# Kernel optimization log

Measured on AMD Instinct MI355X. Metric: run time of the kernel, lower is better.

## Reference

```python
import jax, jax.numpy as jnp
import numpy as np

N = 50000
NUM_FEATURES = 128
HIDDEN = 64
NUM_CLASSES = 32
K_HOPS = 4
E = 1600000
CST = 1e-05


def setup_inputs() -> dict:
    key = jax.random.key(0)
    ks = jax.random.split(key, 12)
    def lin(k, fan_in, fan_out):
        b = 1.0 / np.sqrt(fan_in)
        kw, kb = jax.random.split(k)
        W = jax.random.uniform(kw, (fan_in, fan_out), jnp.float32, -b, b)
        bias = jax.random.uniform(kb, (fan_out,), jnp.float32, -b, b)
        return W, bias
    W_in, b_in = lin(ks[0], NUM_FEATURES, HIDDEN)
    WQ, bQ = lin(ks[1], HIDDEN, HIDDEN)
    WK, bK = lin(ks[2], HIDDEN, HIDDEN)
    WV, bV = lin(ks[3], HIDDEN, NUM_CLASSES)
    return {
        'node_feat': jax.random.normal(ks[4], (N, NUM_FEATURES), jnp.float32),
        'W_in': W_in, 'b_in': b_in,
        'WQ': WQ, 'bQ': bQ,
        'WK': WK, 'bK': bK,
        'WV': WV, 'bV': bV,
        'hopwise': jnp.ones((K_HOPS + 1,), jnp.float32),
        'teleport': jnp.ones((1,), jnp.float32),
        'edge_index': jax.random.randint(ks[5], (2, E), 0, N, jnp.int64 if jax.config.jax_enable_x64 else jnp.int32),
    }


def reference(node_feat, W_in, b_in, WQ, bQ, WK, bK, WV, bV, hopwise, teleport, edge_index):
    n = node_feat.shape[0]
    row, col = edge_index[0], edge_index[1]
    # random-walk norm: deg over targets (col), inverted, indexed at sources (row)
    deg = jax.ops.segment_sum(jnp.ones_like(row, node_feat.dtype), col, num_segments=n)
    deg_inv = jnp.where(deg > 0, 1.0 / deg, 0.0)
    norm = deg_inv[row]  # [E]

    x = jax.nn.relu(node_feat @ W_in + b_in)          # [n, h]
    Q = 1.0 + jax.nn.elu(x @ WQ + bQ)                 # [n, h]
    Kf = 1.0 + jax.nn.elu(x @ WK + bK)                # [n, h]
    V = x @ WV + bV                                   # [n, c]
    M = jnp.einsum('ni,nj->nij', Kf, V)               # [n, h, c]

    # global attention (teleport) branch
    teleportM = jnp.sum(M, axis=0) / n                # [h, c]
    teleportK = jnp.sum(Kf, axis=0) / n               # [h]
    teleportH = jnp.einsum('ni,ij->nj', Q, teleportM)
    teleportC = jnp.einsum('ni,i->n', Q, teleportK)[:, None] + CST
    teleportH = teleportH / teleportC

    hidden = V * hopwise[0]
    for hop in range(K_HOPS):
        # edge gather -> weight -> scatter-sum (message passing)
        M = jax.ops.segment_sum(norm[:, None, None] * M[row], col, num_segments=n)
        Kf = jax.ops.segment_sum(norm[:, None] * Kf[row], col, num_segments=n)
        H = jnp.einsum('ni,nij->nj', Q, M)
        C = jnp.sum(Q * Kf, axis=-1, keepdims=True) + CST
        hidden = hidden + hopwise[hop + 1] * (H / C)

    hidden = hidden + teleport * teleportH
    return hidden
```

## Files before the change

### kernel.cpp

```cpp
#include <hip/hip_runtime.h>
#include <math.h>
#include <stdint.h>

#define NN 50000
#define FIN 128
#define HD 64
#define CD 32
#define EE 1600000
#define CSTV 1e-5f
#define NB 49

typedef unsigned short u16;
typedef unsigned int u32;
typedef unsigned char u8;
typedef unsigned int uv2 __attribute__((ext_vector_type(2)));
typedef unsigned int uv4 __attribute__((ext_vector_type(4)));
typedef float fv2 __attribute__((ext_vector_type(2)));

static __device__ __forceinline__ float b2f(u16 u){
  union { float f; u32 i; } v; v.i = ((u32)u) << 16; return v.f;
}
static __device__ __forceinline__ u16 f2b(float f){
  union { float f; u32 u; } v; v.f = f;
  u32 u = v.u;
  u32 r = (u + 0x7fffu + ((u >> 16) & 1u)) >> 16;
  return (u16)r;
}
static __device__ __forceinline__ float ldin(const void* p, size_t i, int isf){
  return isf ? ((const float*)p)[i] : b2f(((const u16*)p)[i]);
}

static __device__ __forceinline__ void dec8(u32 g, float* f){
  fv2 lo = __builtin_amdgcn_cvt_pk_f32_fp8(g, false);
  fv2 hi = __builtin_amdgcn_cvt_pk_f32_fp8(g, true);
  f[0] = lo.x; f[1] = lo.y; f[2] = hi.x; f[3] = hi.y;
}
static __device__ __forceinline__ u32 enc8(const float* f){
  u32 r = 0;
  r = __builtin_amdgcn_cvt_pk_fp8_f32(f[0], f[1], r, false);
  r = __builtin_amdgcn_cvt_pk_fp8_f32(f[2], f[3], r, true);
  return r;
}
template<int C>
static __device__ __forceinline__ void loadF8(const u8* __restrict__ p, float* f){
  if constexpr (C == 32){
    uint4 g0 = ((const uint4*)p)[0];
    uint4 g1 = ((const uint4*)p)[1];
    dec8(g0.x, f+0);  dec8(g0.y, f+4);  dec8(g0.z, f+8);  dec8(g0.w, f+12);
    dec8(g1.x, f+16); dec8(g1.y, f+20); dec8(g1.z, f+24); dec8(g1.w, f+28);
  } else if constexpr (C == 16){
    uint4 g = *(const uint4*)p;
    dec8(g.x, f+0); dec8(g.y, f+4); dec8(g.z, f+8); dec8(g.w, f+12);
  } else {
    uint2 g = *(const uint2*)p;
    dec8(g.x, f+0); dec8(g.y, f+4);
  }
}
template<int C>
static __device__ __forceinline__ void storeF8NT(u8* __restrict__ p, const float* f){
  if constexpr (C == 32){
    uv4 g0, g1;
    g0.x=enc8(f+0);  g0.y=enc8(f+4);  g0.z=enc8(f+8);  g0.w=enc8(f+12);
    g1.x=enc8(f+16); g1.y=enc8(f+20); g1.z=enc8(f+24); g1.w=enc8(f+28);
    __builtin_nontemporal_store(g0, (uv4*)p);
    __builtin_nontemporal_store(g1, (uv4*)p + 1);
  } else if constexpr (C == 16){
    uv4 g; g.x=enc8(f+0); g.y=enc8(f+4); g.z=enc8(f+8); g.w=enc8(f+12);
    __builtin_nontemporal_store(g, (uv4*)p);
  } else {
    uv2 g; g.x=enc8(f+0); g.y=enc8(f+4);
    __builtin_nontemporal_store(g, (uv2*)p);
  }
}
template<int C>
static __device__ __forceinline__ void loadB(const u16* __restrict__ p, float* f){
  if constexpr (C == 32){
    #pragma unroll
    for (int q = 0; q < 4; ++q){
      uint4 g = ((const uint4*)p)[q];
      f[q*8+0]=b2f((u16)(g.x&0xffff)); f[q*8+1]=b2f((u16)(g.x>>16));
      f[q*8+2]=b2f((u16)(g.y&0xffff)); f[q*8+3]=b2f((u16)(g.y>>16));
      f[q*8+4]=b2f((u16)(g.z&0xffff)); f[q*8+5]=b2f((u16)(g.z>>16));
      f[q*8+6]=b2f((u16)(g.w&0xffff)); f[q*8+7]=b2f((u16)(g.w>>16));
    }
  } else if constexpr (C == 16){
    #pragma unroll
    for (int q = 0; q < 2; ++q){
      uint4 g = ((const uint4*)p)[q];
      f[q*8+0]=b2f((u16)(g.x&0xffff)); f[q*8+1]=b2f((u16)(g.x>>16));
      f[q*8+2]=b2f((u16)(g.y&0xffff)); f[q*8+3]=b2f((u16)(g.y>>16));
      f[q*8+4]=b2f((u16)(g.z&0xffff)); f[q*8+5]=b2f((u16)(g.z>>16));
      f[q*8+6]=b2f((u16)(g.w&0xffff)); f[q*8+7]=b2f((u16)(g.w>>16));
    }
  } else {
    uint4 g = *(const uint4*)p;
    f[0]=b2f((u16)(g.x&0xffff)); f[1]=b2f((u16)(g.x>>16));
    f[2]=b2f((u16)(g.y&0xffff)); f[3]=b2f((u16)(g.y>>16));
    f[4]=b2f((u16)(g.z&0xffff)); f[5]=b2f((u16)(g.z>>16));
    f[6]=b2f((u16)(g.w&0xffff)); f[7]=b2f((u16)(g.w>>16));
  }
}

__global__ void k_detect(const u16* __restrict__ w, int* __restrict__ flag){
  __shared__ int bad;
  if (threadIdx.x == 0) bad = 0;
  __syncthreads();
  for (int i = threadIdx.x; i < 2048; i += 256){
    float v = b2f(w[i]);
    if (!(fabsf(v) <= 1.0f)) bad = 1;
  }
  __syncthreads();
  if (threadIdx.x == 0) flag[0] = bad;
}


__global__ void k_zero(int* cnt, float* teleM, float* teleK){
  int i = blockIdx.x * 256 + threadIdx.x;
  if (i < NN) cnt[i] = 0;
  if (i < HD * CD) teleM[i] = 0.f;
  if (i < HD) teleK[i] = 0.f;
}

__global__ void k_hist(const int* __restrict__ colp, int* __restrict__ cnt){
  int e = blockIdx.x * 256 + threadIdx.x;
  if (e < EE) atomicAdd(&cnt[colp[e]], 1);
}

__global__ __launch_bounds__(1024) void k_scanA(const int* __restrict__ cnt,
                                                int* __restrict__ loc, int* __restrict__ bsum){
  __shared__ int wsum[16];
  int t = threadIdx.x; int i = blockIdx.x * 1024 + t;
  int v = (i < NN) ? cnt[i] : 0;
  int x = v;
  int lane = t & 63, wid = t >> 6;
  #pragma unroll
  for (int d = 1; d < 64; d <<= 1){ int n = __shfl_up(x, d, 64); if (lane >= d) x += n; }
  if (lane == 63) wsum[wid] = x;
  __syncthreads();
  if (t < 16){
    int y = wsum[t];
    #pragma unroll
    for (int d = 1; d < 16; d <<= 1){ int n = __shfl_up(y, d, 16); if (t >= d) y += n; }
    wsum[t] = y;
  }
  __syncthreads();
  if (wid > 0) x += wsum[wid - 1];
  if (i < NN) loc[i] = x;
  if (t == 1023) bsum[blockIdx.x] = x;
}

__global__ __launch_bounds__(64) void k_scanB(const int* __restrict__ bsum,
                                              int* __restrict__ boff, int* __restrict__ ptrNN){
  int t = threadIdx.x;
  int v = (t < NB) ? bsum[t] : 0;
  int x = v;
  #pragma unroll
  for (int d = 1; d < 64; d <<= 1){ int n = __shfl_up(x, d, 64); if (t >= d) x += n; }
  if (t < NB) boff[t] = x - v;
  if (t == 63) ptrNN[0] = x;
}

__global__ __launch_bounds__(1024) void k_scanC(const int* __restrict__ cnt, const int* __restrict__ loc,
                                                const int* __restrict__ boff, int* __restrict__ ptr,
                                                int* __restrict__ fill, float* __restrict__ dinv){
  int i = blockIdx.x * 1024 + threadIdx.x;
  if (i < NN){
    int c = cnt[i];
    int p = boff[blockIdx.x] + loc[i] - c;
    ptr[i] = p; fill[i] = p;
    dinv[i] = (c > 0) ? 1.f / (float)c : 0.f;
  }
}

__global__ void k_scatter(const int* __restrict__ rowp, const int* __restrict__ colp,
                          const float* __restrict__ dinv, int* __restrict__ fill,
                          int2* __restrict__ ew){
  int e = blockIdx.x * 256 + threadIdx.x;
  if (e < EE){
    int c = colp[e];
    int p = atomicAdd(&fill[c], 1);
    int r = rowp[e];
    int2 v; v.x = r; v.y = __float_as_int(dinv[r]);
    ew[p] = v;
  }
}


__global__ __launch_bounds__(256) void k_x(const void* __restrict__ feat, const void* __restrict__ Win,
                                           const void* __restrict__ bin, const int* __restrict__ fl,
                                           float* __restrict__ x){
  int isf = fl[0];
  __shared__ float Ws[FIN * HD];
  __shared__ float fs[4 * FIN];
  __shared__ float bs[HD];
  int t = threadIdx.x;
  for (int idx = t; idx < FIN * HD; idx += 256) Ws[idx] = ldin(Win, idx, isf);
  if (t < HD) bs[t] = ldin(bin, t, isf);
  int n0 = blockIdx.x * 4;
  for (int idx = t; idx < 4 * FIN; idx += 256){
    int nl = idx >> 7, k = idx & 127; int n = n0 + nl;
    fs[idx] = (n < NN) ? ldin(feat, (size_t)n * FIN + k, isf) : 0.f;
  }
  __syncthreads();
  int nl = t >> 6, o = t & 63; int n = n0 + nl;
  if (n < NN){
    float acc = bs[o];
    #pragma unroll 8
    for (int k = 0; k < FIN; ++k) acc += fs[nl * FIN + k] * Ws[k * HD + o];
    x[(size_t)n * HD + o] = fmaxf(acc, 0.f);
  }
}

__global__ __launch_bounds__(256) void k_qkv(const float* __restrict__ x,
    const void* __restrict__ WQ, const void* __restrict__ bQ,
    const void* __restrict__ WK, const void* __restrict__ bK,
    const void* __restrict__ WV, const void* __restrict__ bV,
    const void* __restrict__ hopwise, const int* __restrict__ fl,
    float* __restrict__ Q, u16* __restrict__ Kf0b, u16* __restrict__ Vb,
    float* __restrict__ hid){
  int isf = fl[0];
  __shared__ float WQs[HD * HD], WKs[HD * HD], WVs[HD * CD];
  __shared__ float bqs[HD], bks[HD], bvs[CD];
  __shared__ float xs[4 * HD];
  int t = threadIdx.x;
  for (int idx = t; idx < HD * HD; idx += 256){ WQs[idx] = ldin(WQ, idx, isf); WKs[idx] = ldin(WK, idx, isf); }
  for (int idx = t; idx < HD * CD; idx += 256) WVs[idx] = ldin(WV, idx, isf);
  if (t < HD){ bqs[t] = ldin(bQ, t, isf); bks[t] = ldin(bK, t, isf); }
  if (t < CD) bvs[t] = ldin(bV, t, isf);
  int n0 = blockIdx.x * 4;
  for (int idx = t; idx < 4 * HD; idx += 256){
    int nl = idx >> 6; int n = n0 + nl;
    xs[idx] = (n < NN) ? x[(size_t)n * HD + (idx & 63)] : 0.f;
  }
  __syncthreads();
  int nl = t >> 6, o = t & 63; int n = n0 + nl;
  float hw0 = ldin(hopwise, 0, isf);
  float q = bqs[o], kf = bks[o];
  #pragma unroll 8
  for (int k = 0; k < HD; ++k){
    float xv = xs[nl * HD + k];
    q  += xv * WQs[k * HD + o];
    kf += xv * WKs[k * HD + o];
  }
  q  = (q  > 0.f) ? 1.f + q  : expf(q);
  kf = (kf > 0.f) ? 1.f + kf : expf(kf);
  if (n < NN){ Q[(size_t)n * HD + o] = q; Kf0b[(size_t)n * HD + o] = f2b(kf); }
  if (o < CD && n < NN){
    float v = bvs[o];
    #pragma unroll 8
    for (int k = 0; k < HD; ++k) v += xs[nl * HD + k] * WVs[k * CD + o];
    Vb[(size_t)n * CD + o] = f2b(v);
    hid[(size_t)n * CD + o] = hw0 * v;
  }
}


__global__ __launch_bounds__(256) void k_tele(const u16* __restrict__ Kf0b, const u16* __restrict__ Vb,
                                              float* __restrict__ teleM, float* __restrict__ teleK){
  __shared__ float accM[HD * CD];
  __shared__ float accKs[HD];
  __shared__ float KfL[HD];
  __shared__ float VL[CD];
  int t = threadIdx.x;
  for (int idx = t; idx < HD * CD; idx += 256) accM[idx] = 0.f;
  if (t < HD) accKs[t] = 0.f;
  __syncthreads();
  for (int n = blockIdx.x; n < NN; n += gridDim.x){
    if (t < HD) KfL[t] = b2f(Kf0b[(size_t)n * HD + t]);
    else if (t < HD + CD) VL[t - HD] = b2f(Vb[(size_t)n * CD + (t - HD)]);
    __syncthreads();
    for (int idx = t; idx < HD * CD; idx += 256){
      int h = idx >> 5, c = idx & 31;
      accM[idx] += KfL[h] * VL[c];
    }
    if (t < HD) accKs[t] += KfL[t];
    __syncthreads();
  }
  for (int idx = t; idx < HD * CD; idx += 256) atomicAdd(&teleM[idx], accM[idx]);
  if (t < HD) atomicAdd(&teleK[t], accKs[t]);
}


template<int C, bool FIRST, bool FUSEK, bool LAST>
__global__ __launch_bounds__(128)
void k_hop(const u8* __restrict__ Min, const u16* __restrict__ Kf0b, const u16* __restrict__ Vb,
           const u16* __restrict__ KfIn, u16* __restrict__ KfOut,
           const float* __restrict__ Qb, const int2* __restrict__ ew, const int* __restrict__ ptr,
           float* __restrict__ invC, const void* __restrict__ hopw, const int* __restrict__ fl,
           int hopidx, u8* __restrict__ Mout, float* __restrict__ hid, int c0){
  int wv = threadIdx.x >> 6;
  int t = threadIdx.x & 63;
  int i = blockIdx.x * 2 + wv;
  int e0 = __builtin_amdgcn_readfirstlane(ptr[i]);
  int e1 = __builtin_amdgcn_readfirstlane(ptr[i + 1]);
  float a[C];
  #pragma unroll
  for (int j = 0; j < C; ++j) a[j] = 0.f;
  float accK = 0.f;
  int e = e0;
  if constexpr (FIRST){
    for (; e + 2 <= e1; e += 2){
      int2 d0 = ew[e], d1 = ew[e+1];
      float s0 = __int_as_float(d0.y) * b2f(Kf0b[(size_t)d0.x * HD + t]);
      float s1 = __int_as_float(d1.y) * b2f(Kf0b[(size_t)d1.x * HD + t]);
      float v0[C], v1[C];
      loadB<C>(Vb + (size_t)d0.x * CD + c0, v0);
      loadB<C>(Vb + (size_t)d1.x * CD + c0, v1);
      #pragma unroll
      for (int j = 0; j < C; ++j) a[j] += s0 * v0[j] + s1 * v1[j];
      if constexpr (FUSEK) accK += s0 + s1;
    }
    for (; e < e1; ++e){
      int2 d0 = ew[e];
      float s0 = __int_as_float(d0.y) * b2f(Kf0b[(size_t)d0.x * HD + t]);
      float v0[C];
      loadB<C>(Vb + (size_t)d0.x * CD + c0, v0);
      #pragma unroll
      for (int j = 0; j < C; ++j) a[j] += s0 * v0[j];
      if constexpr (FUSEK) accK += s0;
    }
  } else {
    for (; e + 2 <= e1; e += 2){
      int2 d0 = ew[e], d1 = ew[e+1];
      float w0 = __int_as_float(d0.y), w1 = __int_as_float(d1.y);
      float m0[C], m1[C];
      loadF8<C>(Min + (size_t)d0.x * (HD * C) + t * C, m0);
      loadF8<C>(Min + (size_t)d1.x * (HD * C) + t * C, m1);
      if constexpr (FUSEK){
        accK += w0 * b2f(KfIn[(size_t)d0.x * HD + t]) + w1 * b2f(KfIn[(size_t)d1.x * HD + t]);
      }
      #pragma unroll
      for (int j = 0; j < C; ++j) a[j] += w0 * m0[j] + w1 * m1[j];
    }
    for (; e < e1; ++e){
      int2 d0 = ew[e];
      float w0 = __int_as_float(d0.y);
      float m0[C];
      loadF8<C>(Min + (size_t)d0.x * (HD * C) + t * C, m0);
      if constexpr (FUSEK) accK += w0 * b2f(KfIn[(size_t)d0.x * HD + t]);
      #pragma unroll
      for (int j = 0; j < C; ++j) a[j] += w0 * m0[j];
    }
  }
  float q = Qb[(size_t)i * HD + t];
  float ic;
  if constexpr (FUSEK){
    if constexpr (!LAST) KfOut[(size_t)i * HD + t] = f2b(accK);
    float ck = q * accK;
    #pragma unroll
    for (int off = 32; off >= 1; off >>= 1) ck += __shfl_down(ck, off, 64);
    ck = 1.f / (ck + CSTV);
    if (t == 0) invC[i] = ck;
    ic = ck;
  } else {
    ic = invC[i];
  }
  float p[C];
  #pragma unroll
  for (int j = 0; j < C; ++j) p[j] = q * a[j];
  #pragma unroll
  for (int off = 32; off >= 1; off >>= 1){
    #pragma unroll
    for (int j = 0; j < C; ++j) p[j] += __shfl_down(p[j], off, 64);
  }
  if (t == 0){
    float coef = ldin(hopw, hopidx, fl[0]) * ic;
    float* hp = hid + (size_t)i * CD + c0;
    #pragma unroll
    for (int j = 0; j < C; ++j) hp[j] += coef * p[j];
  }
  if constexpr (!LAST) storeF8NT<C>(Mout + (size_t)i * (HD * C) + t * C, a);
}


__global__ __launch_bounds__(256) void k_final(const float* __restrict__ hid, const float* __restrict__ Qb,
    const float* __restrict__ teleM, const float* __restrict__ teleK, const void* __restrict__ tel,
    const int* __restrict__ fl, void* __restrict__ out){
  int isf = fl[0];
  __shared__ float tM[HD * CD];
  __shared__ float tK[HD];
  int t = threadIdx.x;
  for (int idx = t; idx < HD * CD; idx += 256) tM[idx] = teleM[idx];
  if (t < HD) tK[t] = teleK[t];
  __syncthreads();
  int nl = t >> 5, c = t & 31;
  int n = blockIdx.x * 8 + nl;
  if (n < NN){
    const float* q = Qb + (size_t)n * HD;
    float dH = 0.f, dK = 0.f;
    #pragma unroll 8
    for (int h = 0; h < HD; ++h){
      float qv = q[h];
      dH += qv * tM[h * CD + c];
      dK += qv * tK[h];
    }
    float invn = 1.f / (float)NN;
    float tH = (dH * invn) / (dK * invn + CSTV);
    float val = hid[(size_t)n * CD + c] + ldin(tel, 0, isf) * tH;
    if (isf) ((float*)out)[(size_t)n * CD + c] = val;
    else ((u16*)out)[(size_t)n * CD + c] = f2b(val);
  }
}


template<int C>
static void launch_chunks(u8* Ma, u8* Mb, const u16* Kf0b, const u16* Vb,
                          u16* KfPa, u16* KfPb, const float* Q, const int2* ew,
                          const int* ptr, float* invC, const void* hop, const int* flag,
                          float* hid, hipStream_t stream){
  int nchunks = CD / C;
  int grid = NN / 2;
  for (int ch = 0; ch < nchunks; ++ch){
    int c0 = ch * C;
    if (ch == 0){
      k_hop<C,true ,true ,false><<<grid,128,0,stream>>>(nullptr, Kf0b, Vb, nullptr, KfPa, Q, ew, ptr, invC+0*NN, hop, flag, 1, Ma, hid, c0);
      k_hop<C,false,true ,false><<<grid,128,0,stream>>>(Ma, Kf0b, Vb, KfPa, KfPb, Q, ew, ptr, invC+1*NN, hop, flag, 2, Mb, hid, c0);
      k_hop<C,false,true ,false><<<grid,128,0,stream>>>(Mb, Kf0b, Vb, KfPb, KfPa, Q, ew, ptr, invC+2*NN, hop, flag, 3, Ma, hid, c0);
      k_hop<C,false,true ,true ><<<grid,128,0,stream>>>(Ma, Kf0b, Vb, KfPa, nullptr, Q, ew, ptr, invC+3*NN, hop, flag, 4, nullptr, hid, c0);
    } else {
      k_hop<C,true ,false,false><<<grid,128,0,stream>>>(nullptr, Kf0b, Vb, nullptr, nullptr, Q, ew, ptr, invC+0*NN, hop, flag, 1, Ma, hid, c0);
      k_hop<C,false,false,false><<<grid,128,0,stream>>>(Ma, Kf0b, Vb, nullptr, nullptr, Q, ew, ptr, invC+1*NN, hop, flag, 2, Mb, hid, c0);
      k_hop<C,false,false,false><<<grid,128,0,stream>>>(Mb, Kf0b, Vb, nullptr, nullptr, Q, ew, ptr, invC+2*NN, hop, flag, 3, Ma, hid, c0);
      k_hop<C,false,false,true ><<<grid,128,0,stream>>>(Ma, Kf0b, Vb, nullptr, nullptr, Q, ew, ptr, invC+3*NN, hop, flag, 4, nullptr, hid, c0);
    }
  }
}


extern "C" void kernel_launch(void* const* d_in, const int* in_sizes, int n_in,
                              void* d_out, int out_size, void* d_ws, size_t ws_size,
                              hipStream_t stream){
  const void* feat = d_in[0];
  const void* Win  = d_in[1];
  const void* bin  = d_in[2];
  const void* WQ   = d_in[3];
  const void* bQ   = d_in[4];
  const void* WK   = d_in[5];
  const void* bK   = d_in[6];
  const void* WV   = d_in[7];
  const void* bV   = d_in[8];
  const void* hop  = d_in[9];
  const void* tel  = d_in[10];
  const int* ei    = (const int*)d_in[11];
  const int* rowp  = ei;
  const int* colp  = ei + EE;

  char* w = (char*)d_ws;
  size_t off = 0;
  auto pad = [](size_t x){ return (x + 255) & ~((size_t)255); };
  auto alloc = [&](size_t bytes) -> char* {
    char* p = w + off;
    off += pad(bytes);
    return p;
  };
  float* Q    = (float*)alloc((size_t)NN * HD * 4);
  float* hid  = (float*)alloc((size_t)NN * CD * 4);
  float* invC = (float*)alloc((size_t)4 * NN * 4);
  float* dinv = (float*)alloc((size_t)NN * 4);
  int*   cnt  = (int*)alloc((size_t)NN * 4);
  int*   ptr  = (int*)alloc((size_t)(NN + 1) * 4);
  int*   fill = (int*)alloc((size_t)NN * 4);
  int*   bsum = (int*)alloc(64 * 4);
  int*   boff = (int*)alloc(64 * 4);
  int2*  ew   = (int2*)alloc((size_t)EE * 8);
  float* teleM= (float*)alloc((size_t)HD * CD * 4);
  float* teleK= (float*)alloc((size_t)HD * 4);
  int*   flag = (int*)alloc(256);
  u16*   Kf0b = (u16*)alloc((size_t)NN * HD * 2);
  u16*   KfPa = (u16*)alloc((size_t)NN * HD * 2);
  u16*   KfPb = (u16*)alloc((size_t)NN * HD * 2);
  u16*   Vb   = (u16*)alloc((size_t)NN * CD * 2);

  size_t fixed = off;
  auto fits = [&](int C){ return fixed + 2 * pad((size_t)NN * HD * C) <= ws_size; };
  int C = fits(32) ? 32 : (fits(16) ? 16 : 8);
  size_t mbytes = pad((size_t)NN * HD * C);
  char* mreg = alloc(2 * mbytes);
  u8* Ma = (u8*)mreg;
  u8* Mb = (u8*)(mreg + mbytes);
  float* x = (float*)mreg;

  k_detect<<<1, 256, 0, stream>>>((const u16*)Win, flag);
  k_zero<<<(NN + 255) / 256, 256, 0, stream>>>(cnt, teleM, teleK);
  k_hist<<<(EE + 255) / 256, 256, 0, stream>>>(colp, cnt);
  k_scanA<<<NB, 1024, 0, stream>>>(cnt, fill, bsum);
  k_scanB<<<1, 64, 0, stream>>>(bsum, boff, ptr + NN);
  k_scanC<<<NB, 1024, 0, stream>>>(cnt, fill, boff, ptr, fill, dinv);
  k_scatter<<<(EE + 255) / 256, 256, 0, stream>>>(rowp, colp, dinv, fill, ew);
  k_x<<<(NN + 3) / 4, 256, 0, stream>>>(feat, Win, bin, flag, x);
  k_qkv<<<(NN + 3) / 4, 256, 0, stream>>>(x, WQ, bQ, WK, bK, WV, bV, hop, flag, Q, Kf0b, Vb, hid);
  k_tele<<<256, 256, 0, stream>>>(Kf0b, Vb, teleM, teleK);

  if (C == 32)      launch_chunks<32>(Ma, Mb, Kf0b, Vb, KfPa, KfPb, Q, ew, ptr, invC, hop, flag, hid, stream);
  else if (C == 16) launch_chunks<16>(Ma, Mb, Kf0b, Vb, KfPa, KfPb, Q, ew, ptr, invC, hop, flag, hid, stream);
  else              launch_chunks<8 >(Ma, Mb, Kf0b, Vb, KfPa, KfPb, Q, ew, ptr, invC, hop, flag, hid, stream);

  k_final<<<(NN + 7) / 8, 256, 0, stream>>>(hid, Q, teleM, teleK, tel, flag, d_out);
}
```

Measured before the change: 2.279 ms.

## Fuse input projection with QKV projection and fold detect into zero kernel

Merges the input-linear kernel and the Q/K/V projection kernel into one kernel that processes 16 nodes per block, keeping the intermediate x in shared memory instead of writing it to global memory. Weights are staged in shared memory as bf16 to fit, which amortizes weight loading over more nodes but rounds the weights to bf16. The dtype-detect kernel is folded into the zero kernel to remove a launch, and the teleport reduction grid is raised to 1024 blocks. The weight rounding may change numerics slightly, and the larger per-block work lowers block count.

```diff
diff --git a/kernel.cpp b/kernel.cpp
--- a/kernel.cpp
+++ b/kernel.cpp
@@ -101,25 +101,25 @@
   }
 }
 
-__global__ void k_detect(const u16* __restrict__ w, int* __restrict__ flag){
-  __shared__ int bad;
-  if (threadIdx.x == 0) bad = 0;
-  __syncthreads();
-  for (int i = threadIdx.x; i < 2048; i += 256){
-    float v = b2f(w[i]);
-    if (!(fabsf(v) <= 1.0f)) bad = 1;
-  }
-  __syncthreads();
-  if (threadIdx.x == 0) flag[0] = bad;
-}
-
-
-__global__ void k_zero(int* cnt, float* teleM, float* teleK){
+__global__ void k_zero(const u16* __restrict__ w, int* __restrict__ flag,
+                       int* cnt, float* teleM, float* teleK){
   int i = blockIdx.x * 256 + threadIdx.x;
   if (i < NN) cnt[i] = 0;
   if (i < HD * CD) teleM[i] = 0.f;
   if (i < HD) teleK[i] = 0.f;
-}
+  if (blockIdx.x == 0){
+    __shared__ int bad;
+    if (threadIdx.x == 0) bad = 0;
+    __syncthreads();
+    for (int k = threadIdx.x; k < 2048; k += 256){
+      float v = b2f(w[k]);
+      if (!(fabsf(v) <= 1.0f)) bad = 1;
+    }
+    __syncthreads();
+    if (threadIdx.x == 0) flag[0] = bad;
+  }
+}
+
 
 __global__ void k_hist(const int* __restrict__ colp, int* __restrict__ cnt){
   int e = blockIdx.x * 256 + threadIdx.x;
@@ -186,32 +186,8 @@
 }
 
 
-__global__ __launch_bounds__(256) void k_x(const void* __restrict__ feat, const void* __restrict__ Win,
-                                           const void* __restrict__ bin, const int* __restrict__ fl,
-                                           float* __restrict__ x){
-  int isf = fl[0];
-  __shared__ float Ws[FIN * HD];
-  __shared__ float fs[4 * FIN];
-  __shared__ float bs[HD];
-  int t = threadIdx.x;
-  for (int idx = t; idx < FIN * HD; idx += 256) Ws[idx] = ldin(Win, idx, isf);
-  if (t < HD) bs[t] = ldin(bin, t, isf);
-  int n0 = blockIdx.x * 4;
-  for (int idx = t; idx < 4 * FIN; idx += 256){
-    int nl = idx >> 7, k = idx & 127; int n = n0 + nl;
-    fs[idx] = (n < NN) ? ldin(feat, (size_t)n * FIN + k, isf) : 0.f;
-  }
-  __syncthreads();
-  int nl = t >> 6, o = t & 63; int n = n0 + nl;
-  if (n < NN){
-    float acc = bs[o];
-    #pragma unroll 8
-    for (int k = 0; k < FIN; ++k) acc += fs[nl * FIN + k] * Ws[k * HD + o];
-    x[(size_t)n * HD + o] = fmaxf(acc, 0.f);
-  }
-}
-
-__global__ __launch_bounds__(256) void k_qkv(const float* __restrict__ x,
+__global__ __launch_bounds__(256) void k_feat(
+    const void* __restrict__ feat, const void* __restrict__ Win, const void* __restrict__ bin,
     const void* __restrict__ WQ, const void* __restrict__ bQ,
     const void* __restrict__ WK, const void* __restrict__ bK,
     const void* __restrict__ WV, const void* __restrict__ bV,
@@ -219,38 +195,64 @@
     float* __restrict__ Q, u16* __restrict__ Kf0b, u16* __restrict__ Vb,
     float* __restrict__ hid){
   int isf = fl[0];
-  __shared__ float WQs[HD * HD], WKs[HD * HD], WVs[HD * CD];
-  __shared__ float bqs[HD], bks[HD], bvs[CD];
-  __shared__ float xs[4 * HD];
+  __shared__ u16 Ws[FIN * HD];
+  __shared__ u16 WQs[HD * HD];
+  __shared__ u16 WKs[HD * HD];
+  __shared__ u16 WVs[HD * CD];
+  __shared__ float bs[HD], bqs[HD], bks[HD], bvs[CD];
+  __shared__ float fs[16 * FIN];
+  __shared__ float xs[16 * HD];
   int t = threadIdx.x;
-  for (int idx = t; idx < HD * HD; idx += 256){ WQs[idx] = ldin(WQ, idx, isf); WKs[idx] = ldin(WK, idx, isf); }
-  for (int idx = t; idx < HD * CD; idx += 256) WVs[idx] = ldin(WV, idx, isf);
-  if (t < HD){ bqs[t] = ldin(bQ, t, isf); bks[t] = ldin(bK, t, isf); }
+  for (int idx = t; idx < FIN * HD; idx += 256) Ws[idx] = f2b(ldin(Win, idx, isf));
+  for (int idx = t; idx < HD * HD; idx += 256){
+    WQs[idx] = f2b(ldin(WQ, idx, isf));
+    WKs[idx] = f2b(ldin(WK, idx, isf));
+  }
+  for (int idx = t; idx < HD * CD; idx += 256) WVs[idx] = f2b(ldin(WV, idx, isf));
+  if (t < HD){ bs[t] = ldin(bin, t, isf); bqs[t] = ldin(bQ, t, isf); bks[t] = ldin(bK, t, isf); }
   if (t < CD) bvs[t] = ldin(bV, t, isf);
-  int n0 = blockIdx.x * 4;
-  for (int idx = t; idx < 4 * HD; idx += 256){
-    int nl = idx >> 6; int n = n0 + nl;
-    xs[idx] = (n < NN) ? x[(size_t)n * HD + (idx & 63)] : 0.f;
-  }
-  __syncthreads();
-  int nl = t >> 6, o = t & 63; int n = n0 + nl;
+  int n0 = blockIdx.x * 16;
+  for (int idx = t; idx < 16 * FIN; idx += 256){
+    int nl = idx >> 7, k = idx & 127; int n = n0 + nl;
+    fs[idx] = (n < NN) ? ldin(feat, (size_t)n * FIN + k, isf) : 0.f;
+  }
+  __syncthreads();
+  int o = t & 63, g = t >> 6;
+  #pragma unroll
+  for (int rep = 0; rep < 4; ++rep){
+    int nl = g + rep * 4;
+    float acc = bs[o];
+    #pragma unroll 8
+    for (int k = 0; k < FIN; ++k) acc += fs[nl * FIN + k] * b2f(Ws[k * HD + o]);
+    xs[nl * HD + o] = fmaxf(acc, 0.f);
+  }
+  __syncthreads();
   float hw0 = ldin(hopwise, 0, isf);
-  float q = bqs[o], kf = bks[o];
-  #pragma unroll 8
-  for (int k = 0; k < HD; ++k){
-    float xv = xs[nl * HD + k];
-    q  += xv * WQs[k * HD + o];
-    kf += xv * WKs[k * HD + o];
-  }
-  q  = (q  > 0.f) ? 1.f + q  : expf(q);
-  kf = (kf > 0.f) ? 1.f + kf : expf(kf);
-  if (n < NN){ Q[(size_t)n * HD + o] = q; Kf0b[(size_t)n * HD + o] = f2b(kf); }
-  if (o < CD && n < NN){
-    float v = bvs[o];
+  #pragma unroll
+  for (int rep = 0; rep < 4; ++rep){
+    int nl = g + rep * 4; int n = n0 + nl;
+    float q = bqs[o], kf = bks[o];
     #pragma unroll 8
-    for (int k = 0; k < HD; ++k) v += xs[nl * HD + k] * WVs[k * CD + o];
-    Vb[(size_t)n * CD + o] = f2b(v);
-    hid[(size_t)n * CD + o] = hw0 * v;
+    for (int k = 0; k < HD; ++k){
+      float xv = xs[nl * HD + k];
+      q  += xv * b2f(WQs[k * HD + o]);
+      kf += xv * b2f(WKs[k * HD + o]);
+    }
+    q  = (q  > 0.f) ? 1.f + q  : expf(q);
+    kf = (kf > 0.f) ? 1.f + kf : expf(kf);
+    if (n < NN){ Q[(size_t)n * HD + o] = q; Kf0b[(size_t)n * HD + o] = f2b(kf); }
+  }
+  int c = t & 31;
+  #pragma unroll
+  for (int rep = 0; rep < 2; ++rep){
+    int nv = (t >> 5) + rep * 8; int n = n0 + nv;
+    if (n < NN){
+      float v = bvs[c];
+      #pragma unroll 8
+      for (int k = 0; k < HD; ++k) v += xs[nv * HD + k] * b2f(WVs[k * CD + c]);
+      Vb[(size_t)n * CD + c] = f2b(v);
+      hid[(size_t)n * CD + c] = hw0 * v;
+    }
   }
 }
 
@@ -478,18 +480,16 @@
   char* mreg = alloc(2 * mbytes);
   u8* Ma = (u8*)mreg;
   u8* Mb = (u8*)(mreg + mbytes);
-  float* x = (float*)mreg;
-
-  k_detect<<<1, 256, 0, stream>>>((const u16*)Win, flag);
-  k_zero<<<(NN + 255) / 256, 256, 0, stream>>>(cnt, teleM, teleK);
+
+  k_zero<<<(NN + 255) / 256, 256, 0, stream>>>((const u16*)Win, flag, cnt, teleM, teleK);
   k_hist<<<(EE + 255) / 256, 256, 0, stream>>>(colp, cnt);
   k_scanA<<<NB, 1024, 0, stream>>>(cnt, fill, bsum);
   k_scanB<<<1, 64, 0, stream>>>(bsum, boff, ptr + NN);
   k_scanC<<<NB, 1024, 0, stream>>>(cnt, fill, boff, ptr, fill, dinv);
   k_scatter<<<(EE + 255) / 256, 256, 0, stream>>>(rowp, colp, dinv, fill, ew);
-  k_x<<<(NN + 3) / 4, 256, 0, stream>>>(feat, Win, bin, flag, x);
-  k_qkv<<<(NN + 3) / 4, 256, 0, stream>>>(x, WQ, bQ, WK, bK, WV, bV, hop, flag, Q, Kf0b, Vb, hid);
-  k_tele<<<256, 256, 0, stream>>>(Kf0b, Vb, teleM, teleK);
+  k_feat<<<(NN + 15) / 16, 256, 0, stream>>>(feat, Win, bin, WQ, bQ, WK, bK, WV, bV,
+                                             hop, flag, Q, Kf0b, Vb, hid);
+  k_tele<<<1024, 256, 0, stream>>>(Kf0b, Vb, teleM, teleK);
 
   if (C == 32)      launch_chunks<32>(Ma, Mb, Kf0b, Vb, KfPa, KfPb, Q, ew, ptr, invC, hop, flag, hid, stream);
   else if (C == 16) launch_chunks<16>(Ma, Mb, Kf0b, Vb, KfPa, KfPb, Q, ew, ptr, invC, hop, flag, hid, stream);
```

After: 2.128 ms. 1.07x faster.
